# Kernel optimization log

Measured on AMD Instinct MI355X. Metric: run time of the kernel, lower is better.

## Reference

```python
import jax, jax.numpy as jnp
import numpy as np

B, S, D, DA, DP = 32, 4096, 256, 128, 64


def setup_inputs() -> dict:
    key = jax.random.key(0)
    ks = jax.random.split(key, 10)
    scale = 0.05
    return {
        "h": jax.random.normal(ks[0], (B, S, D), jnp.float32),
        "q": jax.random.normal(ks[1], (B, D), jnp.float32),
        "pf1": jax.random.normal(ks[2], (B, S, DP), jnp.float32),
        "pf2": jax.random.normal(ks[3], (B, S, DP), jnp.float32),
        "Wh": jax.random.normal(ks[4], (DA, D), jnp.float32) * scale,
        "Wq": jax.random.normal(ks[5], (DA, D), jnp.float32) * scale,
        "Wp1": jax.random.normal(ks[6], (DP, DP), jnp.float32) * scale,
        "Wp2": jax.random.normal(ks[7], (DP, DP), jnp.float32) * scale,
        "Wc": jax.random.normal(ks[8], (1, 2 * DA + 2 * DP), jnp.float32) * scale,
        "bc": jax.random.normal(ks[9], (1,), jnp.float32) * scale,
    }


def reference(h, q, pf1, pf2, Wh, Wq, Wp1, Wp2, Wc, bc):
    # h: [B,S,d], q: [B,d], pf1/pf2: [B,S,dp]
    da = Wh.shape[0]
    dp = Wp1.shape[0]
    w = Wc[0]  # [2da+2dp]
    wa, wq, wp1, wp2 = (w[:da], w[da:2 * da], w[2 * da:2 * da + dp], w[2 * da + dp:])
    # context_linear(cat([h_lin, q_lin, pf1_lin, pf2_lin])) decomposes into a sum
    # of per-branch contributions; fuse the two chained matmuls per branch.
    score = (
        h @ (Wh.T @ wa)                 # [B,S]
        + (q @ (Wq.T @ wq))[:, None]    # [B,1] broadcast
        + pf1 @ (Wp1.T @ wp1)           # [B,S]
        + pf2 @ (Wp2.T @ wp2)           # [B,S]
        + bc[0]
    )
    values = jnp.tanh(score)            # dropout is identity in eval
    att = jax.nn.softmax(values, axis=-1)  # [B,S]
    # torch.mean over the stacked S axis -> weighted MEAN, not sum
    context = jnp.einsum('bs,bsd->bd', att, h) / h.shape[1]
    return context
```

## Files before the change

### kernel.cpp

```cpp
#include <hip/hip_runtime.h>
#include <math.h>

#define BB 32
#define SS 4096
#define DD 256
#define DAA 128
#define DPP 64
#define CHUNKS 32
#define ROWS_PER_BLOCK (SS / CHUNKS)
#define WAVES_PER_BLOCK 4
#define ROWS_PER_WAVE (ROWS_PER_BLOCK / WAVES_PER_BLOCK)

#define WS_VH   0
#define WS_VP1  256
#define WS_VP2  320
#define WS_QDOT 384
#define WS_PART 416
#define PART_STRIDE 258

__global__ void prep_kernel(const float* __restrict__ q,
                            const float* __restrict__ Wh,
                            const float* __restrict__ Wq,
                            const float* __restrict__ Wp1,
                            const float* __restrict__ Wp2,
                            const float* __restrict__ Wc,
                            const float* __restrict__ bc,
                            float* __restrict__ ws) {
    __shared__ float s_vq[DD];
    const int tid = threadIdx.x;
    float vh = 0.f, vq = 0.f;
    for (int a = 0; a < DAA; ++a) {
        vh += Wh[a * DD + tid] * Wc[a];
        vq += Wq[a * DD + tid] * Wc[DAA + a];
    }
    ws[WS_VH + tid] = vh;
    s_vq[tid] = vq;
    if (tid < DPP) {
        float vp1 = 0.f, vp2 = 0.f;
        for (int a = 0; a < DPP; ++a) {
            vp1 += Wp1[a * DPP + tid] * Wc[2 * DAA + a];
            vp2 += Wp2[a * DPP + tid] * Wc[2 * DAA + DPP + a];
        }
        ws[WS_VP1 + tid] = vp1;
        ws[WS_VP2 + tid] = vp2;
    }
    __syncthreads();
    if (tid < BB) {
        float acc = bc[0];
        for (int d = 0; d < DD; ++d) acc += q[tid * DD + d] * s_vq[d];
        ws[WS_QDOT + tid] = acc;
    }
}

__global__ __launch_bounds__(256) void
main_kernel(const float* __restrict__ h,
            const float* __restrict__ pf1,
            const float* __restrict__ pf2,
            float* __restrict__ ws) {
    const int c    = blockIdx.x;
    const int b    = blockIdx.y;
    const int tid  = threadIdx.x;
    const int wave = tid >> 6;
    const int lane = tid & 63;

    const float4 vh4  = ((const float4*)(ws + WS_VH))[lane];
    const float  vp1l = ws[WS_VP1 + lane];
    const float  vp2l = ws[WS_VP2 + lane];
    const float  qd   = ws[WS_QDOT + b];

    const int s0 = c * ROWS_PER_BLOCK;
    const float4* hbase  = (const float4*)(h + (size_t)b * SS * DD);
    const float*  p1base = pf1 + (size_t)b * SS * DPP;
    const float*  p2base = pf2 + (size_t)b * SS * DPP;

    float  m = -INFINITY, l = 0.f;
    float4 ctx = make_float4(0.f, 0.f, 0.f, 0.f);

    for (int i = 0; i < ROWS_PER_WAVE; ++i) {
        const int s = s0 + i * WAVES_PER_BLOCK + wave;
        const float4 h4 = hbase[(size_t)s * (DD / 4) + lane];
        const float  p1 = p1base[s * DPP + lane];
        const float  p2 = p2base[s * DPP + lane];

        float part = h4.x * vh4.x + h4.y * vh4.y + h4.z * vh4.z + h4.w * vh4.w
                   + p1 * vp1l + p2 * vp2l;
        #pragma unroll
        for (int off = 32; off >= 1; off >>= 1)
            part += __shfl_xor(part, off, 64);

        const float score = part + qd;
        const float e2 = __expf(2.f * score);
        const float t  = (e2 - 1.f) / (e2 + 1.f);

        const float mn = fmaxf(m, t);
        const float sc = __expf(m - mn);
        const float w  = __expf(t - mn);
        l = l * sc + w;
        ctx.x = ctx.x * sc + w * h4.x;
        ctx.y = ctx.y * sc + w * h4.y;
        ctx.z = ctx.z * sc + w * h4.z;
        ctx.w = ctx.w * sc + w * h4.w;
        m = mn;
    }

    __shared__ float s_m[WAVES_PER_BLOCK], s_l[WAVES_PER_BLOCK];
    __shared__ float s_ctx[WAVES_PER_BLOCK][DD];
    if (lane == 0) { s_m[wave] = m; s_l[wave] = l; }
    ((float4*)s_ctx[wave])[lane] = ctx;
    __syncthreads();

    const float M  = fmaxf(fmaxf(s_m[0], s_m[1]), fmaxf(s_m[2], s_m[3]));
    const float f0 = __expf(s_m[0] - M), f1 = __expf(s_m[1] - M);
    const float f2 = __expf(s_m[2] - M), f3 = __expf(s_m[3] - M);
    const float L  = f0 * s_l[0] + f1 * s_l[1] + f2 * s_l[2] + f3 * s_l[3];
    const float cd = f0 * s_ctx[0][tid] + f1 * s_ctx[1][tid]
                   + f2 * s_ctx[2][tid] + f3 * s_ctx[3][tid];

    float* part_out = ws + WS_PART + (size_t)(b * CHUNKS + c) * PART_STRIDE;
    if (tid == 0) { part_out[0] = M; part_out[1] = L; }
    part_out[2 + tid] = cd;
}

__global__ void finalize_kernel(const float* __restrict__ ws,
                                float* __restrict__ out) {
    const int b   = blockIdx.x;
    const int tid = threadIdx.x;
    __shared__ float s_m[CHUNKS], s_l[CHUNKS];
    const float* base = ws + WS_PART + (size_t)b * CHUNKS * PART_STRIDE;
    if (tid < CHUNKS) {
        s_m[tid] = base[(size_t)tid * PART_STRIDE + 0];
        s_l[tid] = base[(size_t)tid * PART_STRIDE + 1];
    }
    __syncthreads();
    float M = -INFINITY;
    #pragma unroll
    for (int c = 0; c < CHUNKS; ++c) M = fmaxf(M, s_m[c]);
    float L = 0.f, acc = 0.f;
    for (int c = 0; c < CHUNKS; ++c) {
        const float f = __expf(s_m[c] - M);
        L   += f * s_l[c];
        acc += f * base[(size_t)c * PART_STRIDE + 2 + tid];
    }
    out[b * DD + tid] = acc / (L * (float)SS);
}

extern "C" void kernel_launch(void* const* d_in, const int* in_sizes, int n_in,
                              void* d_out, int out_size, void* d_ws, size_t ws_size,
                              hipStream_t stream) {
    const float* h   = (const float*)d_in[0];
    const float* q   = (const float*)d_in[1];
    const float* pf1 = (const float*)d_in[2];
    const float* pf2 = (const float*)d_in[3];
    const float* Wh  = (const float*)d_in[4];
    const float* Wq  = (const float*)d_in[5];
    const float* Wp1 = (const float*)d_in[6];
    const float* Wp2 = (const float*)d_in[7];
    const float* Wc  = (const float*)d_in[8];
    const float* bc  = (const float*)d_in[9];
    float* out = (float*)d_out;
    float* ws  = (float*)d_ws;

    prep_kernel<<<1, 256, 0, stream>>>(q, Wh, Wq, Wp1, Wp2, Wc, bc, ws);
    main_kernel<<<dim3(CHUNKS, BB), 256, 0, stream>>>(h, pf1, pf2, ws);
    finalize_kernel<<<BB, 256, 0, stream>>>(ws, out);
}
```

Measured before the change: 273.3 us.

## Drop online-softmax max tracking, batch row loads, and accumulate partials via atomics

Because tanh bounds scores to [-1,1], the softmax no longer tracks a running max; exp weights are summed directly and block partials are combined with atomicAdd into a zeroed workspace, so the finalize step becomes a single divide. Each wave now handles a contiguous run of rows and loads four rows before reducing, which gives more memory-level parallelism and interleaves the shuffle reductions. Chunks double to 64 for more blocks, launch bounds request higher occupancy, and the q·vq dot moves into the main kernel. The trade-offs are atomic contention and non-deterministic float summation order.

```diff
diff --git a/kernel.cpp b/kernel.cpp
--- a/kernel.cpp
+++ b/kernel.cpp
@@ -6,54 +6,56 @@
 #define DD 256
 #define DAA 128
 #define DPP 64
-#define CHUNKS 32
+#define CHUNKS 64
 #define ROWS_PER_BLOCK (SS / CHUNKS)
 #define WAVES_PER_BLOCK 4
 #define ROWS_PER_WAVE (ROWS_PER_BLOCK / WAVES_PER_BLOCK)
+#define BATCH 4
+#define NBATCH (ROWS_PER_WAVE / BATCH)
 
 #define WS_VH   0
-#define WS_VP1  256
-#define WS_VP2  320
-#define WS_QDOT 384
-#define WS_PART 416
-#define PART_STRIDE 258
+#define WS_VQ   256
+#define WS_VP1  512
+#define WS_VP2  576
+#define WS_BC   640
+#define WS_ACC  656
+#define WS_LSUM (WS_ACC + BB * DD)
+#define WS_ZERO_N (BB * DD + BB)
 
-__global__ void prep_kernel(const float* __restrict__ q,
-                            const float* __restrict__ Wh,
+__global__ void prep_kernel(const float* __restrict__ Wh,
                             const float* __restrict__ Wq,
                             const float* __restrict__ Wp1,
                             const float* __restrict__ Wp2,
                             const float* __restrict__ Wc,
                             const float* __restrict__ bc,
                             float* __restrict__ ws) {
-    __shared__ float s_vq[DD];
     const int tid = threadIdx.x;
-    float vh = 0.f, vq = 0.f;
-    for (int a = 0; a < DAA; ++a) {
-        vh += Wh[a * DD + tid] * Wc[a];
-        vq += Wq[a * DD + tid] * Wc[DAA + a];
-    }
-    ws[WS_VH + tid] = vh;
-    s_vq[tid] = vq;
-    if (tid < DPP) {
-        float vp1 = 0.f, vp2 = 0.f;
-        for (int a = 0; a < DPP; ++a) {
-            vp1 += Wp1[a * DPP + tid] * Wc[2 * DAA + a];
-            vp2 += Wp2[a * DPP + tid] * Wc[2 * DAA + DPP + a];
+    if (blockIdx.x == 0) {
+        float vh = 0.f, vq = 0.f;
+        for (int a = 0; a < DAA; ++a) {
+            vh += Wh[a * DD + tid] * Wc[a];
+            vq += Wq[a * DD + tid] * Wc[DAA + a];
         }
-        ws[WS_VP1 + tid] = vp1;
-        ws[WS_VP2 + tid] = vp2;
-    }
-    __syncthreads();
-    if (tid < BB) {
-        float acc = bc[0];
-        for (int d = 0; d < DD; ++d) acc += q[tid * DD + d] * s_vq[d];
-        ws[WS_QDOT + tid] = acc;
+        ws[WS_VH + tid] = vh;
+        ws[WS_VQ + tid] = vq;
+        if (tid < DPP) {
+            float vp1 = 0.f, vp2 = 0.f;
+            for (int a = 0; a < DPP; ++a) {
+                vp1 += Wp1[a * DPP + tid] * Wc[2 * DAA + a];
+                vp2 += Wp2[a * DPP + tid] * Wc[2 * DAA + DPP + a];
+            }
+            ws[WS_VP1 + tid] = vp1;
+            ws[WS_VP2 + tid] = vp2;
+        }
+        if (tid == 0) ws[WS_BC] = bc[0];
+    } else {
+        for (int i = tid; i < WS_ZERO_N; i += 256) ws[WS_ACC + i] = 0.f;
     }
 }
 
-__global__ __launch_bounds__(256) void
+__global__ __launch_bounds__(256, 8) void
 main_kernel(const float* __restrict__ h,
+            const float* __restrict__ q,
             const float* __restrict__ pf1,
             const float* __restrict__ pf2,
             float* __restrict__ ws) {
@@ -66,82 +68,77 @@
     const float4 vh4  = ((const float4*)(ws + WS_VH))[lane];
     const float  vp1l = ws[WS_VP1 + lane];
     const float  vp2l = ws[WS_VP2 + lane];
-    const float  qd   = ws[WS_QDOT + b];
 
-    const int s0 = c * ROWS_PER_BLOCK;
+    const float4 q4  = ((const float4*)(q + (size_t)b * DD))[lane];
+    const float4 vq4 = ((const float4*)(ws + WS_VQ))[lane];
+    float qp = q4.x * vq4.x + q4.y * vq4.y + q4.z * vq4.z + q4.w * vq4.w;
+    #pragma unroll
+    for (int off = 32; off >= 1; off >>= 1) qp += __shfl_xor(qp, off, 64);
+    const float qd = qp + ws[WS_BC];
+
+    const int s0 = c * ROWS_PER_BLOCK + wave * ROWS_PER_WAVE;
     const float4* hbase  = (const float4*)(h + (size_t)b * SS * DD);
     const float*  p1base = pf1 + (size_t)b * SS * DPP;
     const float*  p2base = pf2 + (size_t)b * SS * DPP;
 
-    float  m = -INFINITY, l = 0.f;
+    float  l = 0.f;
     float4 ctx = make_float4(0.f, 0.f, 0.f, 0.f);
 
-    for (int i = 0; i < ROWS_PER_WAVE; ++i) {
-        const int s = s0 + i * WAVES_PER_BLOCK + wave;
-        const float4 h4 = hbase[(size_t)s * (DD / 4) + lane];
-        const float  p1 = p1base[s * DPP + lane];
-        const float  p2 = p2base[s * DPP + lane];
-
-        float part = h4.x * vh4.x + h4.y * vh4.y + h4.z * vh4.z + h4.w * vh4.w
-                   + p1 * vp1l + p2 * vp2l;
+    for (int ib = 0; ib < NBATCH; ++ib) {
+        const int sb = s0 + ib * BATCH;
+        float4 h4[BATCH];
+        float  p1[BATCH], p2[BATCH], part[BATCH];
         #pragma unroll
-        for (int off = 32; off >= 1; off >>= 1)
-            part += __shfl_xor(part, off, 64);
-
-        const float score = part + qd;
-        const float e2 = __expf(2.f * score);
-        const float t  = (e2 - 1.f) / (e2 + 1.f);
-
-        const float mn = fmaxf(m, t);
-        const float sc = __expf(m - mn);
-        const float w  = __expf(t - mn);
-        l = l * sc + w;
-        ctx.x = ctx.x * sc + w * h4.x;
-        ctx.y = ctx.y * sc + w * h4.y;
-        ctx.z = ctx.z * sc + w * h4.z;
-        ctx.w = ctx.w * sc + w * h4.w;
-        m = mn;
+        for (int j = 0; j < BATCH; ++j) {
+            const int s = sb + j;
+            h4[j] = hbase[(size_t)s * (DD / 4) + lane];
+            p1[j] = p1base[(size_t)s * DPP + lane];
+            p2[j] = p2base[(size_t)s * DPP + lane];
+        }
+        #pragma unroll
+        for (int j = 0; j < BATCH; ++j) {
+            part[j] = h4[j].x * vh4.x + h4[j].y * vh4.y
+                    + h4[j].z * vh4.z + h4[j].w * vh4.w
+                    + p1[j] * vp1l + p2[j] * vp2l;
+        }
+        #pragma unroll
+        for (int off = 32; off >= 1; off >>= 1) {
+            #pragma unroll
+            for (int j = 0; j < BATCH; ++j)
+                part[j] += __shfl_xor(part[j], off, 64);
+        }
+        #pragma unroll
+        for (int j = 0; j < BATCH; ++j) {
+            const float score = part[j] + qd;
+            const float e2 = __expf(2.f * score);
+            const float t  = 1.f - 2.f * __builtin_amdgcn_rcpf(e2 + 1.f);
+            const float w  = __expf(t);
+            l += w;
+            ctx.x += w * h4[j].x;
+            ctx.y += w * h4[j].y;
+            ctx.z += w * h4[j].z;
+            ctx.w += w * h4[j].w;
+        }
     }
 
-    __shared__ float s_m[WAVES_PER_BLOCK], s_l[WAVES_PER_BLOCK];
+    __shared__ float s_l[WAVES_PER_BLOCK];
     __shared__ float s_ctx[WAVES_PER_BLOCK][DD];
-    if (lane == 0) { s_m[wave] = m; s_l[wave] = l; }
+    if (lane == 0) s_l[wave] = l;
     ((float4*)s_ctx[wave])[lane] = ctx;
     __syncthreads();
 
-    const float M  = fmaxf(fmaxf(s_m[0], s_m[1]), fmaxf(s_m[2], s_m[3]));
-    const float f0 = __expf(s_m[0] - M), f1 = __expf(s_m[1] - M);
-    const float f2 = __expf(s_m[2] - M), f3 = __expf(s_m[3] - M);
-    const float L  = f0 * s_l[0] + f1 * s_l[1] + f2 * s_l[2] + f3 * s_l[3];
-    const float cd = f0 * s_ctx[0][tid] + f1 * s_ctx[1][tid]
-                   + f2 * s_ctx[2][tid] + f3 * s_ctx[3][tid];
-
-    float* part_out = ws + WS_PART + (size_t)(b * CHUNKS + c) * PART_STRIDE;
-    if (tid == 0) { part_out[0] = M; part_out[1] = L; }
-    part_out[2 + tid] = cd;
+    const float cd = s_ctx[0][tid] + s_ctx[1][tid] + s_ctx[2][tid] + s_ctx[3][tid];
+    atomicAdd(&ws[WS_ACC + b * DD + tid], cd);
+    if (tid == 0)
+        atomicAdd(&ws[WS_LSUM + b], s_l[0] + s_l[1] + s_l[2] + s_l[3]);
 }
 
 __global__ void finalize_kernel(const float* __restrict__ ws,
                                 float* __restrict__ out) {
     const int b   = blockIdx.x;
     const int tid = threadIdx.x;
-    __shared__ float s_m[CHUNKS], s_l[CHUNKS];
-    const float* base = ws + WS_PART + (size_t)b * CHUNKS * PART_STRIDE;
-    if (tid < CHUNKS) {
-        s_m[tid] = base[(size_t)tid * PART_STRIDE + 0];
-        s_l[tid] = base[(size_t)tid * PART_STRIDE + 1];
-    }
-    __syncthreads();
-    float M = -INFINITY;
-    #pragma unroll
-    for (int c = 0; c < CHUNKS; ++c) M = fmaxf(M, s_m[c]);
-    float L = 0.f, acc = 0.f;
-    for (int c = 0; c < CHUNKS; ++c) {
-        const float f = __expf(s_m[c] - M);
-        L   += f * s_l[c];
-        acc += f * base[(size_t)c * PART_STRIDE + 2 + tid];
-    }
-    out[b * DD + tid] = acc / (L * (float)SS);
+    out[b * DD + tid] = ws[WS_ACC + b * DD + tid]
+                      / (ws[WS_LSUM + b] * (float)SS);
 }
 
 extern "C" void kernel_launch(void* const* d_in, const int* in_sizes, int n_in,
@@ -160,7 +157,7 @@
     float* out = (float*)d_out;
     float* ws  = (float*)d_ws;
 
-    prep_kernel<<<1, 256, 0, stream>>>(q, Wh, Wq, Wp1, Wp2, Wc, bc, ws);
-    main_kernel<<<dim3(CHUNKS, BB), 256, 0, stream>>>(h, pf1, pf2, ws);
+    prep_kernel<<<2, 256, 0, stream>>>(Wh, Wq, Wp1, Wp2, Wc, bc, ws);
+    main_kernel<<<dim3(CHUNKS, BB), 256, 0, stream>>>(h, q, pf1, pf2, ws);
     finalize_kernel<<<BB, 256, 0, stream>>>(ws, out);
 }
```

New measurement: 349.9 us. +28.0%, slower.
